# Performance work log

Measured on AMD Instinct MI355X. Metric: run time of the kernel, lower is better.

Reference implementation:

```python
import jax, jax.numpy as jnp
import numpy as np


def setup_inputs() -> dict:
    key = jax.random.key(0)
    k1, k2, k3 = jax.random.split(key, 3)
    B, N, D = 16, 2048, 128
    q = jax.random.normal(k1, (B, N, D), dtype=jnp.float32)
    k = jax.random.normal(k2, (B, D, N), dtype=jnp.float32)
    v = jax.random.normal(k3, (B, N, D), dtype=jnp.float32)
    return {"q": q, "k": k, "v": v}


def reference(q, k, v):
    # scores: [B, N, N] — note NO 1/sqrt(d) scaling, matching the source
    scores = jnp.einsum('bnd,bdm->bnm', q, k)
    probs = jax.nn.softmax(scores, axis=-1)
    out = jnp.einsum('bnm,bmd->bnd', probs, v)  # [B, N, D]
    return out
```

## Files before the change

kernel.cpp:

```cpp
#include <hip/hip_runtime.h>


typedef __attribute__((ext_vector_type(8))) _Float16 f16x8;
typedef __attribute__((ext_vector_type(16))) float f32x16;

constexpr int Bz = 16;
constexpr int Nn = 2048;
constexpr int Dd = 128;
constexpr int BM = 128;
constexpr int BN = 32;

__device__ __forceinline__ int swz(int r) { return (r ^ (r >> 3)) & 7; }
__device__ __forceinline__ int sw4(int d) { return ((d >> 1) ^ (d >> 3)) & 3; }

__device__ __forceinline__ uint pkrtz(float a, float b) {
    return __builtin_bit_cast(uint, __builtin_amdgcn_cvt_pkrtz(a, b));
}

__device__ __forceinline__ float exp2i(float x) {
    return __builtin_amdgcn_exp2f(x);
}

__global__ __launch_bounds__(512, 2)
void fattn_kernel(const float* __restrict__ qg,
                  const float* __restrict__ kg,
                  const float* __restrict__ vg,
                  float* __restrict__ og)
{
    __shared__ ushort lds_k[2][BN * Dd];
    __shared__ ushort lds_v[2][Dd * BN];

    const int bid  = blockIdx.x;
    const int xcd  = bid & 7;
    const int idx  = bid >> 3;
    const int b    = xcd * 2 + (idx >> 4);
    const int q0   = (idx & 15) * BM;
    const int tid  = threadIdx.x;
    const int wv   = tid >> 6;
    const int lane = tid & 63;
    const int h    = lane >> 5;
    const int l31  = lane & 31;
    const bool producer = (wv >= 4);

    const int ptid = (wv - 4) * 64 + lane;
    const int kgrp = ptid & 3;
    const int krow = ptid >> 2;
    const int vgrp = ptid & 15;
    const int vrow = ptid >> 4;
    const float* kbase = kg + (size_t)b * Dd * Nn;
    const float* vbase = vg + (size_t)b * Nn * Dd;
    float4 kr0[4], vr0[4], kr1[4], vr1[4];

    auto issue_loads = [&](int n0, float4 (&kr)[4], float4 (&vr)[4]) {
        const int d0 = krow * 2;
        const float* s0 = kbase + (size_t)d0 * Nn + n0 + kgrp * 8;
        kr[0] = ((const float4*)s0)[0];
        kr[1] = ((const float4*)s0)[1];
        kr[2] = ((const float4*)(s0 + Nn))[0];
        kr[3] = ((const float4*)(s0 + Nn))[1];
        const int kk0 = vrow * 2;
        const float* t0 = vbase + (size_t)(n0 + kk0) * Dd + vgrp * 8;
        vr[0] = ((const float4*)t0)[0];
        vr[1] = ((const float4*)t0)[1];
        vr[2] = ((const float4*)(t0 + Dd))[0];
        vr[3] = ((const float4*)(t0 + Dd))[1];
    };
    auto write_lds = [&](int buf, const float4 (&kr)[4], const float4 (&vr)[4]) {
        uint* kw = (uint*)lds_k[buf];
        const float* av = (const float*)&kr[0];
        const float* bv = (const float*)&kr[2];
        #pragma unroll
        for (int j = 0; j < 8; ++j) {
            const int n = kgrp * 8 + j;
            kw[n * (Dd / 2) + (krow ^ (swz(n) << 2))] = pkrtz(av[j], bv[j]);
        }
        uint* vw = (uint*)lds_v[buf];
        const float* cv = (const float*)&vr[0];
        const float* dv = (const float*)&vr[2];
        #pragma unroll
        for (int j = 0; j < 8; ++j) {
            const int dd = vgrp * 8 + j;
            vw[dd * (BN / 2) + (vrow ^ (sw4(dd) << 2))] = pkrtz(cv[j], dv[j]);
        }
    };

    f16x8 qf[8];
    if (!producer) {
        const float* qp = qg + (size_t)(b * Nn + q0 + wv * 32 + l31) * Dd + h * 8;
        #pragma unroll
        for (int c = 0; c < 8; ++c) {
            float4 x0 = *(const float4*)(qp + c * 16);
            float4 x1 = *(const float4*)(qp + c * 16 + 4);
            const float xv[8] = {x0.x, x0.y, x0.z, x0.w, x1.x, x1.y, x1.z, x1.w};
            union { f16x8 v; _Float16 e[8]; } u;
            #pragma unroll
            for (int j = 0; j < 8; ++j)
                u.e[j] = (_Float16)(xv[j] * 1.44269504088896340736f);
            qf[c] = u.v;
        }
    }
    f32x16 accO[4];
    #pragma unroll
    for (int dt = 0; dt < 4; ++dt)
        #pragma unroll
        for (int r = 0; r < 16; ++r) accO[dt][r] = 0.f;
    float m_i = -1e30f, l_i = 0.f;

    auto consume = [&](const ushort* kb, const ushort* vb) {
        f32x16 accS;
        #pragma unroll
        for (int r = 0; r < 16; ++r) accS[r] = 0.f;
        {
            const int kkrow = l31;
            const int sw = swz(kkrow) << 3;
            __builtin_amdgcn_s_setprio(1);
            #pragma unroll
            for (int c = 0; c < 8; ++c) {
                f16x8 kf = *(const f16x8*)&kb[kkrow * Dd + ((c * 16 + h * 8) ^ sw)];
                accS = __builtin_amdgcn_mfma_f32_32x32x16_f16(kf, qf[c], accS, 0, 0, 0);
            }
            __builtin_amdgcn_s_setprio(0);
        }

        f16x8 vf[4][2];
        #pragma unroll
        for (int dt = 0; dt < 4; ++dt) {
            const int drow = dt * 32 + l31;
            const int sv = sw4(drow) << 3;
            vf[dt][0] = *(const f16x8*)&vb[drow * BN + ((8 * h) ^ sv)];
            vf[dt][1] = *(const f16x8*)&vb[drow * BN + ((16 + 8 * h) ^ sv)];
        }

        float t0 = fmaxf(accS[0], accS[1]),  t1 = fmaxf(accS[2], accS[3]);
        float t2 = fmaxf(accS[4], accS[5]),  t3 = fmaxf(accS[6], accS[7]);
        float t4 = fmaxf(accS[8], accS[9]),  t5 = fmaxf(accS[10], accS[11]);
        float t6 = fmaxf(accS[12], accS[13]), t7 = fmaxf(accS[14], accS[15]);
        float u0 = fmaxf(t0, t1), u1 = fmaxf(t2, t3);
        float u2 = fmaxf(t4, t5), u3 = fmaxf(t6, t7);
        float mx = fmaxf(fmaxf(u0, u1), fmaxf(u2, u3));
        mx = fmaxf(mx, __shfl_xor(mx, 32, 64));

        if (!__all(mx <= m_i + 8.f)) {
            const float mn = fmaxf(m_i, mx);
            const float al = exp2i(m_i - mn);
            m_i = mn;
            l_i *= al;
            #pragma unroll
            for (int dt = 0; dt < 4; ++dt)
                #pragma unroll
                for (int r = 0; r < 16; ++r) accO[dt][r] *= al;
        }
        float local = 0.f;
        #pragma unroll
        for (int r = 0; r < 16; ++r) {
            const float p = exp2i(accS[r] - m_i);
            accS[r] = p;
            local += p;
        }
        l_i += local;

        const uint pA0 = pkrtz(accS[0],  accS[1]);
        const uint pA1 = pkrtz(accS[2],  accS[3]);
        const uint pB0 = pkrtz(accS[4],  accS[5]);
        const uint pB1 = pkrtz(accS[6],  accS[7]);
        const uint pC0 = pkrtz(accS[8],  accS[9]);
        const uint pC1 = pkrtz(accS[10], accS[11]);
        const uint pD0 = pkrtz(accS[12], accS[13]);
        const uint pD1 = pkrtz(accS[14], accS[15]);
        const uint yA0 = __shfl_xor(pA0, 32, 64);
        const uint yA1 = __shfl_xor(pA1, 32, 64);
        const uint yB0 = __shfl_xor(pB0, 32, 64);
        const uint yB1 = __shfl_xor(pB1, 32, 64);
        const uint yC0 = __shfl_xor(pC0, 32, 64);
        const uint yC1 = __shfl_xor(pC1, 32, 64);
        const uint yD0 = __shfl_xor(pD0, 32, 64);
        const uint yD1 = __shfl_xor(pD1, 32, 64);
        union { uint u[4]; f16x8 v; } P0, P1;
        P0.u[0] = h ? yB0 : pA0;
        P0.u[1] = h ? yB1 : pA1;
        P0.u[2] = h ? pB0 : yA0;
        P0.u[3] = h ? pB1 : yA1;
        P1.u[0] = h ? yD0 : pC0;
        P1.u[1] = h ? yD1 : pC1;
        P1.u[2] = h ? pD0 : yC0;
        P1.u[3] = h ? pD1 : yC1;
        const f16x8 pf0 = P0.v, pf1 = P1.v;

        __builtin_amdgcn_s_setprio(1);
        #pragma unroll
        for (int dt = 0; dt < 4; ++dt) {
            accO[dt] = __builtin_amdgcn_mfma_f32_32x32x16_f16(vf[dt][0], pf0, accO[dt], 0, 0, 0);
            accO[dt] = __builtin_amdgcn_mfma_f32_32x32x16_f16(vf[dt][1], pf1, accO[dt], 0, 0, 0);
        }
        __builtin_amdgcn_s_setprio(0);
    };

    if (producer) {
        issue_loads(0,  kr0, vr0);
        issue_loads(BN, kr1, vr1);
        write_lds(0, kr0, vr0);
    }
    __syncthreads();

    constexpr int ITERS = Nn / BN;
    for (int it = 0; it < ITERS; it += 2) {
        if (producer) {
            write_lds(1, kr1, vr1);
            if (it + 2 < ITERS) issue_loads((it + 2) * BN, kr0, vr0);
        } else {
            consume(lds_k[0], lds_v[0]);
        }
        __syncthreads();
        if (producer) {
            if (it + 2 < ITERS) write_lds(0, kr0, vr0);
            if (it + 3 < ITERS) issue_loads((it + 3) * BN, kr1, vr1);
        } else {
            consume(lds_k[1], lds_v[1]);
        }
        __syncthreads();
    }

    if (!producer) {
        float l = l_i + __shfl_xor(l_i, 32, 64);
        const float inv = 1.f / l;
        float* ob = og + (size_t)(b * Nn + q0 + wv * 32 + l31) * Dd;
        #pragma unroll
        for (int dt = 0; dt < 4; ++dt) {
            #pragma unroll
            for (int g = 0; g < 4; ++g) {
                float4 val;
                val.x = accO[dt][4 * g + 0] * inv;
                val.y = accO[dt][4 * g + 1] * inv;
                val.z = accO[dt][4 * g + 2] * inv;
                val.w = accO[dt][4 * g + 3] * inv;
                *(float4*)(ob + dt * 32 + 8 * g + 4 * h) = val;
            }
        }
    }
}

extern "C" void kernel_launch(void* const* d_in, const int* in_sizes, int n_in,
                              void* d_out, int out_size, void* d_ws, size_t ws_size,
                              hipStream_t stream) {
    const float* q = (const float*)d_in[0];
    const float* k = (const float*)d_in[1];
    const float* v = (const float*)d_in[2];
    float* o = (float*)d_out;
    (void)d_ws; (void)ws_size; (void)in_sizes; (void)n_in; (void)out_size;
    fattn_kernel<<<dim3(Bz * (Nn / BM)), dim3(512), 0, stream>>>(q, k, v, o);
}
```

Baseline: 133.5 us.

## Software-pipeline QK^T of next tile with softmax and PV of previous tile

Splits the consumer body into a QK^T stage (which also loads the V fragments) and a finish stage (softmax plus PV). The loop is restructured with a prologue and epilogue so each step computes the scores for the current tile while finishing the previous one. The goal is to let the MFMA work of one tile overlap the exp/max VALU work of another. The cost is a second score accumulator and a second set of V fragments held in registers, which raises VGPR pressure under launch_bounds(512,2) and could cause spills.

```diff
diff --git a/kernel.cpp b/kernel.cpp
--- a/kernel.cpp
+++ b/kernel.cpp
@@ -106,23 +106,8 @@
         for (int r = 0; r < 16; ++r) accO[dt][r] = 0.f;
     float m_i = -1e30f, l_i = 0.f;
 
-    auto consume = [&](const ushort* kb, const ushort* vb) {
-        f32x16 accS;
-        #pragma unroll
-        for (int r = 0; r < 16; ++r) accS[r] = 0.f;
-        {
-            const int kkrow = l31;
-            const int sw = swz(kkrow) << 3;
-            __builtin_amdgcn_s_setprio(1);
-            #pragma unroll
-            for (int c = 0; c < 8; ++c) {
-                f16x8 kf = *(const f16x8*)&kb[kkrow * Dd + ((c * 16 + h * 8) ^ sw)];
-                accS = __builtin_amdgcn_mfma_f32_32x32x16_f16(kf, qf[c], accS, 0, 0, 0);
-            }
-            __builtin_amdgcn_s_setprio(0);
-        }
-
-        f16x8 vf[4][2];
+    auto qkt = [&](const ushort* kb, const ushort* vb,
+                   f32x16& accS, f16x8 (&vf)[4][2]) {
         #pragma unroll
         for (int dt = 0; dt < 4; ++dt) {
             const int drow = dt * 32 + l31;
@@ -130,7 +115,20 @@
             vf[dt][0] = *(const f16x8*)&vb[drow * BN + ((8 * h) ^ sv)];
             vf[dt][1] = *(const f16x8*)&vb[drow * BN + ((16 + 8 * h) ^ sv)];
         }
-
+        #pragma unroll
+        for (int r = 0; r < 16; ++r) accS[r] = 0.f;
+        const int kkrow = l31;
+        const int sw = swz(kkrow) << 3;
+        __builtin_amdgcn_s_setprio(1);
+        #pragma unroll
+        for (int c = 0; c < 8; ++c) {
+            f16x8 kf = *(const f16x8*)&kb[kkrow * Dd + ((c * 16 + h * 8) ^ sw)];
+            accS = __builtin_amdgcn_mfma_f32_32x32x16_f16(kf, qf[c], accS, 0, 0, 0);
+        }
+        __builtin_amdgcn_s_setprio(0);
+    };
+
+    auto finish = [&](f32x16& accS, const f16x8 (&vf)[4][2]) {
         float t0 = fmaxf(accS[0], accS[1]),  t1 = fmaxf(accS[2], accS[3]);
         float t2 = fmaxf(accS[4], accS[5]),  t3 = fmaxf(accS[6], accS[7]);
         float t4 = fmaxf(accS[8], accS[9]),  t5 = fmaxf(accS[10], accS[11]);
@@ -195,6 +193,9 @@
         __builtin_amdgcn_s_setprio(0);
     };
 
+    f32x16 sA, sB;
+    f16x8 vfA[4][2], vfB[4][2];
+
     if (producer) {
         issue_loads(0,  kr0, vr0);
         issue_loads(BN, kr1, vr1);
@@ -203,22 +204,41 @@
     __syncthreads();
 
     constexpr int ITERS = Nn / BN;
-    for (int it = 0; it < ITERS; it += 2) {
+    if (producer) {
+        write_lds(1, kr1, vr1);
+        issue_loads(2 * BN, kr0, vr0);
+    } else {
+        qkt(lds_k[0], lds_v[0], sA, vfA);
+    }
+    __syncthreads();
+    if (producer) {
+        write_lds(0, kr0, vr0);
+        issue_loads(3 * BN, kr1, vr1);
+    } else {
+        qkt(lds_k[1], lds_v[1], sB, vfB);
+        finish(sA, vfA);
+    }
+    __syncthreads();
+
+    for (int it = 2; it < ITERS; it += 2) {
         if (producer) {
             write_lds(1, kr1, vr1);
             if (it + 2 < ITERS) issue_loads((it + 2) * BN, kr0, vr0);
         } else {
-            consume(lds_k[0], lds_v[0]);
+            qkt(lds_k[0], lds_v[0], sA, vfA);
+            finish(sB, vfB);
         }
         __syncthreads();
         if (producer) {
             if (it + 2 < ITERS) write_lds(0, kr0, vr0);
             if (it + 3 < ITERS) issue_loads((it + 3) * BN, kr1, vr1);
         } else {
-            consume(lds_k[1], lds_v[1]);
+            qkt(lds_k[1], lds_v[1], sB, vfB);
+            finish(sA, vfA);
         }
         __syncthreads();
     }
+    if (!producer) finish(sB, vfB);
 
     if (!producer) {
         float l = l_i + __shfl_xor(l_i, 32, 64);
```

Measured after the change: 280.0 us. 2.1x slower.

## Split KV range across two wave groups and merge partial softmax results

Applied to the files above, without the earlier changes.

Replaces the producer/consumer warp specialization with two groups of four waves. Each group loads its own half of the key/value sequence, computes on it, and keeps separate double-buffered LDS tiles. At the end, group 1 writes its partial accumulators and max/sum statistics to shared memory, and group 0 rescales both parts and combines them before storing. This doubles the waves doing MFMA work and halves the sequential loop length. In exchange, each wave now issues global loads itself with less prefetch depth, and LDS use and the final merge cost increase.

```diff
diff --git a/kernel.cpp b/kernel.cpp
--- a/kernel.cpp
+++ b/kernel.cpp
@@ -9,6 +9,7 @@
 constexpr int Dd = 128;
 constexpr int BM = 128;
 constexpr int BN = 32;
+constexpr int ITG = (Nn / 2) / BN;
 
 __device__ __forceinline__ int swz(int r) { return (r ^ (r >> 3)) & 7; }
 __device__ __forceinline__ int sw4(int d) { return ((d >> 1) ^ (d >> 3)) & 3; }
@@ -27,8 +28,9 @@
                   const float* __restrict__ vg,
                   float* __restrict__ og)
 {
-    __shared__ ushort lds_k[2][BN * Dd];
-    __shared__ ushort lds_v[2][Dd * BN];
+    __shared__ ushort lds_k[2][2][BN * Dd];
+    __shared__ ushort lds_v[2][2][Dd * BN];
+    __shared__ float  mlx[4][2][32];
 
     const int bid  = blockIdx.x;
     const int xcd  = bid & 7;
@@ -40,18 +42,20 @@
     const int lane = tid & 63;
     const int h    = lane >> 5;
     const int l31  = lane & 31;
-    const bool producer = (wv >= 4);
-
-    const int ptid = (wv - 4) * 64 + lane;
-    const int kgrp = ptid & 3;
-    const int krow = ptid >> 2;
-    const int vgrp = ptid & 15;
-    const int vrow = ptid >> 4;
+    const int grp  = wv >> 2;
+    const int wq   = wv & 3;
+    const int n_base = grp * (Nn / 2);
+
+    const int gtid = wq * 64 + lane;
+    const int kgrp = gtid & 3;
+    const int krow = gtid >> 2;
+    const int vgrp = gtid & 15;
+    const int vrow = gtid >> 4;
     const float* kbase = kg + (size_t)b * Dd * Nn;
     const float* vbase = vg + (size_t)b * Nn * Dd;
-    float4 kr0[4], vr0[4], kr1[4], vr1[4];
-
-    auto issue_loads = [&](int n0, float4 (&kr)[4], float4 (&vr)[4]) {
+    float4 kr[4], vr[4];
+
+    auto issue_loads = [&](int n0) {
         const int d0 = krow * 2;
         const float* s0 = kbase + (size_t)d0 * Nn + n0 + kgrp * 8;
         kr[0] = ((const float4*)s0)[0];
@@ -65,8 +69,8 @@
         vr[2] = ((const float4*)(t0 + Dd))[0];
         vr[3] = ((const float4*)(t0 + Dd))[1];
     };
-    auto write_lds = [&](int buf, const float4 (&kr)[4], const float4 (&vr)[4]) {
-        uint* kw = (uint*)lds_k[buf];
+    auto write_lds = [&](int buf) {
+        uint* kw = (uint*)lds_k[grp][buf];
         const float* av = (const float*)&kr[0];
         const float* bv = (const float*)&kr[2];
         #pragma unroll
@@ -74,7 +78,7 @@
             const int n = kgrp * 8 + j;
             kw[n * (Dd / 2) + (krow ^ (swz(n) << 2))] = pkrtz(av[j], bv[j]);
         }
-        uint* vw = (uint*)lds_v[buf];
+        uint* vw = (uint*)lds_v[grp][buf];
         const float* cv = (const float*)&vr[0];
         const float* dv = (const float*)&vr[2];
         #pragma unroll
@@ -85,8 +89,8 @@
     };
 
     f16x8 qf[8];
-    if (!producer) {
-        const float* qp = qg + (size_t)(b * Nn + q0 + wv * 32 + l31) * Dd + h * 8;
+    {
+        const float* qp = qg + (size_t)(b * Nn + q0 + wq * 32 + l31) * Dd + h * 8;
         #pragma unroll
         for (int c = 0; c < 8; ++c) {
             float4 x0 = *(const float4*)(qp + c * 16);
@@ -111,24 +115,14 @@
         #pragma unroll
         for (int r = 0; r < 16; ++r) accS[r] = 0.f;
         {
-            const int kkrow = l31;
-            const int sw = swz(kkrow) << 3;
+            const int sw = swz(l31) << 3;
             __builtin_amdgcn_s_setprio(1);
             #pragma unroll
             for (int c = 0; c < 8; ++c) {
-                f16x8 kf = *(const f16x8*)&kb[kkrow * Dd + ((c * 16 + h * 8) ^ sw)];
+                f16x8 kf = *(const f16x8*)&kb[l31 * Dd + ((c * 16 + h * 8) ^ sw)];
                 accS = __builtin_amdgcn_mfma_f32_32x32x16_f16(kf, qf[c], accS, 0, 0, 0);
             }
             __builtin_amdgcn_s_setprio(0);
-        }
-
-        f16x8 vf[4][2];
-        #pragma unroll
-        for (int dt = 0; dt < 4; ++dt) {
-            const int drow = dt * 32 + l31;
-            const int sv = sw4(drow) << 3;
-            vf[dt][0] = *(const f16x8*)&vb[drow * BN + ((8 * h) ^ sv)];
-            vf[dt][1] = *(const f16x8*)&vb[drow * BN + ((16 + 8 * h) ^ sv)];
         }
 
         float t0 = fmaxf(accS[0], accS[1]),  t1 = fmaxf(accS[2], accS[3]);
@@ -158,6 +152,15 @@
             local += p;
         }
         l_i += local;
+
+        f16x8 vf[4][2];
+        #pragma unroll
+        for (int dt = 0; dt < 4; ++dt) {
+            const int drow = dt * 32 + l31;
+            const int sv = sw4(drow) << 3;
+            vf[dt][0] = *(const f16x8*)&vb[drow * BN + ((8 * h) ^ sv)];
+            vf[dt][1] = *(const f16x8*)&vb[drow * BN + ((16 + 8 * h) ^ sv)];
+        }
 
         const uint pA0 = pkrtz(accS[0],  accS[1]);
         const uint pA1 = pkrtz(accS[2],  accS[3]);
@@ -195,47 +198,66 @@
         __builtin_amdgcn_s_setprio(0);
     };
 
-    if (producer) {
-        issue_loads(0,  kr0, vr0);
-        issue_loads(BN, kr1, vr1);
-        write_lds(0, kr0, vr0);
-    }
+    issue_loads(n_base);
+    write_lds(0);
+    issue_loads(n_base + BN);
     __syncthreads();
 
-    constexpr int ITERS = Nn / BN;
-    for (int it = 0; it < ITERS; it += 2) {
-        if (producer) {
-            write_lds(1, kr1, vr1);
-            if (it + 2 < ITERS) issue_loads((it + 2) * BN, kr0, vr0);
-        } else {
-            consume(lds_k[0], lds_v[0]);
-        }
-        __syncthreads();
-        if (producer) {
-            if (it + 2 < ITERS) write_lds(0, kr0, vr0);
-            if (it + 3 < ITERS) issue_loads((it + 3) * BN, kr1, vr1);
-        } else {
-            consume(lds_k[1], lds_v[1]);
-        }
-        __syncthreads();
-    }
-
-    if (!producer) {
-        float l = l_i + __shfl_xor(l_i, 32, 64);
-        const float inv = 1.f / l;
-        float* ob = og + (size_t)(b * Nn + q0 + wv * 32 + l31) * Dd;
-        #pragma unroll
-        for (int dt = 0; dt < 4; ++dt) {
-            #pragma unroll
-            for (int g = 0; g < 4; ++g) {
-                float4 val;
-                val.x = accO[dt][4 * g + 0] * inv;
-                val.y = accO[dt][4 * g + 1] * inv;
-                val.z = accO[dt][4 * g + 2] * inv;
-                val.w = accO[dt][4 * g + 3] * inv;
-                *(float4*)(ob + dt * 32 + 8 * g + 4 * h) = val;
+    for (int it = 0; it < ITG; it += 2) {
+        write_lds(1);
+        if (it + 2 < ITG) issue_loads(n_base + (it + 2) * BN);
+        consume(lds_k[grp][0], lds_v[grp][0]);
+        __syncthreads();
+        if (it + 2 < ITG) write_lds(0);
+        if (it + 3 < ITG) issue_loads(n_base + (it + 3) * BN);
+        consume(lds_k[grp][1], lds_v[grp][1]);
+        __syncthreads();
+    }
+
+    float l_full = l_i + __shfl_xor(l_i, 32, 64);
+    const int pair = wq;
+    if (grp == 1 && h == 0) {
+        mlx[pair][0][l31] = m_i;
+        mlx[pair][1][l31] = l_full;
+    }
+    float* sc = (float*)lds_k;
+
+    #pragma unroll
+    for (int rnd = 0; rnd < 2; ++rnd) {
+        if (grp == 1 && (pair >> 1) == rnd) {
+            float* base = sc + (pair & 1) * 4096 + lane * 64;
+            #pragma unroll
+            for (int dt = 0; dt < 4; ++dt)
+                #pragma unroll
+                for (int r = 0; r < 16; ++r)
+                    base[(dt * 16 + r) ^ l31] = accO[dt][r];
+        }
+        __syncthreads();
+        if (grp == 0 && (pair >> 1) == rnd) {
+            const float m_B = mlx[pair][0][l31];
+            const float l_B = mlx[pair][1][l31];
+            const float ms  = fmaxf(m_i, m_B);
+            const float aA  = exp2i(m_i - ms);
+            const float aB  = exp2i(m_B - ms);
+            const float inv = 1.f / (aA * l_full + aB * l_B);
+            const float* base = sc + (pair & 1) * 4096 + lane * 64;
+            float* ob = og + (size_t)(b * Nn + q0 + wq * 32 + l31) * Dd;
+            #pragma unroll
+            for (int dt = 0; dt < 4; ++dt) {
+                #pragma unroll
+                for (int g = 0; g < 4; ++g) {
+                    float4 val;
+                    #pragma unroll
+                    for (int j = 0; j < 4; ++j) {
+                        const int r = 4 * g + j;
+                        const float o = aA * accO[dt][r] + aB * base[(dt * 16 + r) ^ l31];
+                        ((float*)&val)[j] = o * inv;
+                    }
+                    *(float4*)(ob + dt * 32 + 8 * g + 4 * h) = val;
+                }
             }
         }
+        __syncthreads();
     }
 }
 
```

Result: slower. 136.3 us (+2.1%).
